# Performance work log

Measured on AMD Instinct MI355X. Metric: run time of the kernel, lower is better.

The kernel has to match this reference:

```python
import jax, jax.numpy as jnp
import numpy as np

HIDDEN = 1024
NUM_HEADS = 16
HEAD_SIZE = HIDDEN // NUM_HEADS
B, S = 2, 2048


def setup_inputs() -> dict:
    key = jax.random.key(0)
    k_x, k_wqkv, k_bqkv, k_wo, k_bo = jax.random.split(key, 5)
    x = jax.random.normal(k_x, (B, S, HIDDEN), dtype=jnp.float32)
    # Dense kernels, fan-in scaled like lecun_normal init
    Wqkv = jax.random.normal(k_wqkv, (HIDDEN, 3 * HIDDEN), dtype=jnp.float32) / np.sqrt(HIDDEN)
    bqkv = jnp.zeros((3 * HIDDEN,), dtype=jnp.float32)
    Wo = jax.random.normal(k_wo, (HIDDEN, HIDDEN), dtype=jnp.float32) / np.sqrt(HIDDEN)
    bo = jnp.zeros((HIDDEN,), dtype=jnp.float32)
    return {"x": x, "Wqkv": Wqkv, "bqkv": bqkv, "Wo": Wo, "bo": bo}


def reference(x, Wqkv, bqkv, Wo, bo):
    b, s, h = x.shape
    qkv = jnp.einsum('bsh,hf->bsf', x, Wqkv) + bqkv          # [b, s, 3*h]
    qkv = qkv.reshape(b, s, 3, NUM_HEADS, HEAD_SIZE)
    q, k, v = qkv[:, :, 0], qkv[:, :, 1], qkv[:, :, 2]        # [b, s, nh, hd]
    scale = 1.0 / np.sqrt(HEAD_SIZE)
    scores = jnp.einsum('bqhd,bkhd->bhqk', q, k) * scale      # [b, nh, s, s]
    weights = jax.nn.softmax(scores, axis=-1)
    attn = jnp.einsum('bhqk,bkhd->bqhd', weights, v)          # [b, s, nh, hd]
    attn = attn.reshape(b, s, h)
    return jnp.einsum('bsh,hf->bsf', attn, Wo) + bo
```

## Files before the change

kernel.cpp:

```cpp
#include <hip/hip_runtime.h>
#include <hip/hip_bf16.h>

#define HIDDEN 1024
#define NH 16
#define BATCH 2
#define SEQ 2048

typedef __attribute__((ext_vector_type(8))) short bf16x8;
typedef __attribute__((ext_vector_type(4))) float f32x4;

__device__ __forceinline__ ushort f2bf(float f) {
    __hip_bfloat16 h = __float2bfloat16(f);
    return *reinterpret_cast<ushort*>(&h);
}
__device__ __forceinline__ float fexp2(float x) {
#if __has_builtin(__builtin_amdgcn_exp2f)
    return __builtin_amdgcn_exp2f(x);
#else
    return exp2f(x);
#endif
}
__device__ __forceinline__ uint pack_bf_trunc(float a, float b) {
    return __builtin_amdgcn_perm(__float_as_uint(b), __float_as_uint(a), 0x07060302u);
}

__device__ __forceinline__ void async_copy16(const ushort* g, ushort* l) {
    __builtin_amdgcn_global_load_lds((const __attribute__((address_space(1))) void*)g,
                                     (__attribute__((address_space(3))) void*)l,
                                     16, 0, 0);
}

__global__ void prep_kernel(const float* __restrict__ x,
                            const float* __restrict__ Wqkv,
                            const float* __restrict__ Wo,
                            ushort* __restrict__ xb,
                            ushort* __restrict__ Wt,
                            ushort* __restrict__ WoT)
{
    __shared__ float t[32][33];
    const int bid = blockIdx.x;
    const int tid = threadIdx.x;

    if (bid < 4096) {
        int i = (bid * 256 + tid) * 4;
        float4 v = *(const float4*)(x + i);
        ushort4 w;
        w.x = f2bf(v.x); w.y = f2bf(v.y); w.z = f2bf(v.z); w.w = f2bf(v.w);
        *(ushort4*)(xb + i) = w;
        return;
    }
    const int r = tid >> 3;
    const int c = (tid & 7) * 4;
    if (bid < 7168) {
        int tt = bid - 4096;
        int k0 = (tt & 31) * 32;
        int n0 = (tt >> 5) * 32;
        const int N = 3 * HIDDEN, K = HIDDEN;
        float4 v = *(const float4*)(Wqkv + (size_t)(k0 + r) * N + n0 + c);
        t[r][c] = v.x; t[r][c + 1] = v.y; t[r][c + 2] = v.z; t[r][c + 3] = v.w;
        __syncthreads();
        ushort4 w;
        w.x = f2bf(t[c + 0][r]); w.y = f2bf(t[c + 1][r]);
        w.z = f2bf(t[c + 2][r]); w.w = f2bf(t[c + 3][r]);
        *(ushort4*)(Wt + (size_t)(n0 + r) * K + k0 + c) = w;
    } else {
        int tt = bid - 7168;
        int k0 = (tt & 31) * 32;
        int n0 = (tt >> 5) * 32;
        const int N = HIDDEN, K = HIDDEN;
        float4 v = *(const float4*)(Wo + (size_t)(k0 + r) * N + n0 + c);
        t[r][c] = v.x; t[r][c + 1] = v.y; t[r][c + 2] = v.z; t[r][c + 3] = v.w;
        __syncthreads();
        ushort4 w;
        w.x = f2bf(t[c + 0][r]); w.y = f2bf(t[c + 1][r]);
        w.z = f2bf(t[c + 2][r]); w.w = f2bf(t[c + 3][r]);
        *(ushort4*)(WoT + (size_t)(n0 + r) * K + k0 + c) = w;
    }
}

__global__ __launch_bounds__(256, 3)
void gemm_mfma_bf16_kernel(const ushort* __restrict__ A,
                           const ushort* __restrict__ Bt,
                           const float* __restrict__ bias,
                           ushort* __restrict__ C, int N,
                           int qscale_cols, float qscale,
                           ushort* __restrict__ vtg, int vt_mode)
{
    constexpr int K = 1024;
    __shared__ ushort As[128 * 64];
    __shared__ ushort Bs[128 * 64];

    const int tid  = threadIdx.x;
    const int wave = tid >> 6;
    const int lane = tid & 63;
    const int l16  = lane & 15;
    const int quad = lane >> 4;
    const int wm = wave & 1, wn = wave >> 1;

    const int bm = blockIdx.y * 128;
    const int bn = blockIdx.x * 128;

    const int srow = lane >> 3;
    const int lblk = (lane & 7) ^ srow;
    const ushort* Ag = A  + (size_t)(bm + wave * 32 + srow) * K + lblk * 8;
    const ushort* Bg = Bt + (size_t)(bn + wave * 32 + srow) * K + lblk * 8;
    ushort* Asl = As + wave * 32 * 64;
    ushort* Bsl = Bs + wave * 32 * 64;

    f32x4 acc[4][4];
    #pragma unroll
    for (int i = 0; i < 4; i++)
        #pragma unroll
        for (int j = 0; j < 4; j++) acc[i][j] = (f32x4){0.f, 0.f, 0.f, 0.f};

    for (int k0 = 0; k0 < K; k0 += 64) {
        __syncthreads();
        #pragma unroll
        for (int t = 0; t < 4; t++) {
            async_copy16(Ag + (size_t)t * 8 * K + k0, Asl + t * 8 * 64);
            async_copy16(Bg + (size_t)t * 8 * K + k0, Bsl + t * 8 * 64);
        }
        __syncthreads();

        #pragma unroll
        for (int s = 0; s < 2; s++) {
            bf16x8 af[4], bfr[4];
            #pragma unroll
            for (int i = 0; i < 4; i++) {
                int m = wm * 64 + i * 16 + l16;
                int n = wn * 64 + i * 16 + l16;
                af[i]  = *(const bf16x8*)&As[m * 64 + (((s * 4 + quad) ^ (m & 7)) << 3)];
                bfr[i] = *(const bf16x8*)&Bs[n * 64 + (((s * 4 + quad) ^ (n & 7)) << 3)];
            }
            #pragma unroll
            for (int i = 0; i < 4; i++)
                #pragma unroll
                for (int j = 0; j < 4; j++)
                    acc[i][j] = __builtin_amdgcn_mfma_f32_16x16x32_bf16(af[i], bfr[j], acc[i][j], 0, 0, 0);
        }
    }

    #pragma unroll
    for (int j = 0; j < 4; j++) {
        int col = bn + wn * 64 + j * 16 + l16;
        float bv = bias[col];
        if (vt_mode && col >= 2048) {
            int dfull = col - 2048;
            int hh = dfull >> 6, dd = dfull & 63;
            int bb = bm >> 11;
            int sb = ((bm & 2047) + wm * 64) >> 6;
            ushort tmp[16];
            #pragma unroll
            for (int i = 0; i < 4; i++)
                #pragma unroll
                for (int r = 0; r < 4; r++)
                    tmp[r * 4 + i] = f2bf(acc[i][j][r] + bv);
            ushort* dst = vtg + ((size_t)((bb * NH + hh) * 64 + dd)) * SEQ
                          + sb * 64 + quad * 16;
            *(uint4*)dst = *(const uint4*)tmp;
            *(uint4*)(dst + 8) = *(const uint4*)(tmp + 8);
        } else {
            float s = (col < qscale_cols) ? qscale : 1.0f;
            #pragma unroll
            for (int i = 0; i < 4; i++) {
                int row0 = bm + wm * 64 + i * 16 + quad * 4;
                #pragma unroll
                for (int r = 0; r < 4; r++)
                    C[(size_t)(row0 + r) * N + col] = f2bf((acc[i][j][r] + bv) * s);
            }
        }
    }
}

__global__ __launch_bounds__(256, 4)
void gemm_out_kernel(const ushort* __restrict__ A,
                     const ushort* __restrict__ Bt,
                     const float* __restrict__ bias,
                     float* __restrict__ C)
{
    constexpr int K = 1024, N = 1024;
    __shared__ ushort As[128 * 64];
    __shared__ ushort Bs[64 * 64];

    const int tid  = threadIdx.x;
    const int wave = tid >> 6;
    const int lane = tid & 63;
    const int l16  = lane & 15;
    const int quad = lane >> 4;
    const int wm = wave & 1, wn = wave >> 1;

    const int bm = blockIdx.y * 128;
    const int bn = blockIdx.x * 64;

    const int srow = lane >> 3;
    const int lblk = (lane & 7) ^ srow;
    const ushort* Ag = A  + (size_t)(bm + wave * 32 + srow) * K + lblk * 8;
    const ushort* Bg = Bt + (size_t)(bn + wave * 16 + srow) * K + lblk * 8;
    ushort* Asl = As + wave * 32 * 64;
    ushort* Bsl = Bs + wave * 16 * 64;

    f32x4 acc[4][2];
    #pragma unroll
    for (int i = 0; i < 4; i++)
        #pragma unroll
        for (int j = 0; j < 2; j++) acc[i][j] = (f32x4){0.f, 0.f, 0.f, 0.f};

    for (int k0 = 0; k0 < K; k0 += 64) {
        __syncthreads();
        #pragma unroll
        for (int t = 0; t < 4; t++)
            async_copy16(Ag + (size_t)t * 8 * K + k0, Asl + t * 8 * 64);
        #pragma unroll
        for (int t = 0; t < 2; t++)
            async_copy16(Bg + (size_t)t * 8 * K + k0, Bsl + t * 8 * 64);
        __syncthreads();

        #pragma unroll
        for (int s = 0; s < 2; s++) {
            bf16x8 af[4], bfr[2];
            #pragma unroll
            for (int i = 0; i < 4; i++) {
                int m = wm * 64 + i * 16 + l16;
                af[i] = *(const bf16x8*)&As[m * 64 + (((s * 4 + quad) ^ (m & 7)) << 3)];
            }
            #pragma unroll
            for (int j = 0; j < 2; j++) {
                int n = wn * 32 + j * 16 + l16;
                bfr[j] = *(const bf16x8*)&Bs[n * 64 + (((s * 4 + quad) ^ (n & 7)) << 3)];
            }
            #pragma unroll
            for (int i = 0; i < 4; i++)
                #pragma unroll
                for (int j = 0; j < 2; j++)
                    acc[i][j] = __builtin_amdgcn_mfma_f32_16x16x32_bf16(af[i], bfr[j], acc[i][j], 0, 0, 0);
        }
    }

    #pragma unroll
    for (int j = 0; j < 2; j++) {
        int col = bn + wn * 32 + j * 16 + l16;
        float bv = bias[col];
        #pragma unroll
        for (int i = 0; i < 4; i++) {
            int row0 = bm + wm * 64 + i * 16 + quad * 4;
            #pragma unroll
            for (int r = 0; r < 4; r++)
                C[(size_t)(row0 + r) * N + col] = acc[i][j][r] + bv;
        }
    }
}

__global__ __launch_bounds__(256, 2)
void attn_mfma_v6_kernel(const ushort* __restrict__ qkvb,
                         const ushort* __restrict__ vtg,
                         ushort* __restrict__ attn)
{
    __shared__ __align__(16) ushort smem[34816];

    const int tid  = threadIdx.x;
    const int wave = tid >> 6;
    const int qg   = wave & 1;
    const int kh   = wave >> 1;
    const int lane = tid & 63;
    const int l16  = lane & 15;
    const int quad = lane >> 4;

    const int qb = blockIdx.x & 15;
    const int bh = blockIdx.x >> 4;
    const int h  = bh & (NH - 1);
    const int b  = bh >> 4;

    const int qbase = qb * 128 + qg * 64;
    const int hoff  = h * 64;

    ushort* KsH = smem + kh * 4096;
    ushort* VsH = smem + 8192 + kh * 4096;
    ushort* Psw = smem + 16384 + wave * 4608;

    bf16x8 a_q[4][2];
    #pragma unroll
    for (int mg = 0; mg < 4; mg++) {
        int qrow = b * SEQ + qbase + mg * 16 + l16;
        const ushort* qp = qkvb + (size_t)qrow * 3072 + hoff + quad * 8;
        a_q[mg][0] = *(const bf16x8*)qp;
        a_q[mg][1] = *(const bf16x8*)(qp + 32);
    }

    f32x4 o[4][4];
    f32x4 lacc[4];
    #pragma unroll
    for (int mg = 0; mg < 4; mg++) {
        lacc[mg] = (f32x4){0.f, 0.f, 0.f, 0.f};
        #pragma unroll
        for (int nt = 0; nt < 4; nt++) o[mg][nt] = (f32x4){0.f, 0.f, 0.f, 0.f};
    }

    bf16x8 b_ones;
    #pragma unroll
    for (int j = 0; j < 8; j++) b_ones[j] = (short)0x3f80;

    const ushort* kvb    = qkvb + (size_t)b * SEQ * 3072;
    const ushort* vtg_bh = vtg + (size_t)((b * NH + h) * 64) * SEQ;

    const int srow8 = lane >> 3;
    const int gblk  = ((lane & 7) ^ srow8) << 3;
    const ushort* kg = kvb + (size_t)(kh * 1024 + qg * 32 + srow8) * 3072 + 1024 + hoff + gblk;
    const ushort* vg = vtg_bh + (size_t)(qg * 32 + srow8) * SEQ + kh * 1024 + gblk;

    for (int t = 0; t < 16; t++) {
        const int k0 = t * 64;
        __syncthreads();
        #pragma unroll
        for (int c = 0; c < 4; c++) {
            async_copy16(kg + (size_t)(k0 + c * 8) * 3072, KsH + (qg * 32 + c * 8) * 64);
            async_copy16(vg + (size_t)(c * 8) * SEQ + k0,  VsH + (qg * 32 + c * 8) * 64);
        }
        __syncthreads();

        f32x4 sc[4][4];
        #pragma unroll
        for (int nt = 0; nt < 4; nt++) {
            int key = nt * 16 + l16;
            bf16x8 bk0 = *(const bf16x8*)&KsH[key * 64 + ((quad ^ (key & 7)) << 3)];
            bf16x8 bk1 = *(const bf16x8*)&KsH[key * 64 + (((4 + quad) ^ (key & 7)) << 3)];
            #pragma unroll
            for (int mg = 0; mg < 4; mg++) {
                f32x4 a = (f32x4){0.f, 0.f, 0.f, 0.f};
                a = __builtin_amdgcn_mfma_f32_16x16x32_bf16(a_q[mg][0], bk0, a, 0, 0, 0);
                a = __builtin_amdgcn_mfma_f32_16x16x32_bf16(a_q[mg][1], bk1, a, 0, 0, 0);
                sc[mg][nt] = a;
            }
        }

        #pragma unroll
        for (int mg = 0; mg < 4; mg++) {
            #pragma unroll
            for (int r = 0; r < 4; r++) {
                int q = mg * 16 + quad * 4 + r;
                uint2 pk2;
                pk2.x = pack_bf_trunc(fexp2(sc[mg][0][r]), fexp2(sc[mg][1][r]));
                pk2.y = pack_bf_trunc(fexp2(sc[mg][2][r]), fexp2(sc[mg][3][r]));
                *(uint2*)&Psw[q * 72 + l16 * 4] = pk2;
            }
        }

        asm volatile("s_waitcnt lgkmcnt(0)" ::: "memory");

        #pragma unroll
        for (int mg = 0; mg < 4; mg++) {
            bf16x8 ap0 = *(const bf16x8*)&Psw[(mg * 16 + l16) * 72 + quad * 8];
            bf16x8 ap1 = *(const bf16x8*)&Psw[(mg * 16 + l16) * 72 + 32 + quad * 8];
            #pragma unroll
            for (int nt = 0; nt < 4; nt++) {
                int d = nt * 16 + l16;
                bf16x8 bv0 = *(const bf16x8*)&VsH[d * 64 + ((quad ^ (d & 7)) << 3)];
                bf16x8 bv1 = *(const bf16x8*)&VsH[d * 64 + (((4 + quad) ^ (d & 7)) << 3)];
                o[mg][nt] = __builtin_amdgcn_mfma_f32_16x16x32_bf16(ap0, bv0, o[mg][nt], 0, 0, 0);
                o[mg][nt] = __builtin_amdgcn_mfma_f32_16x16x32_bf16(ap1, bv1, o[mg][nt], 0, 0, 0);
            }
            lacc[mg] = __builtin_amdgcn_mfma_f32_16x16x32_bf16(ap0, b_ones, lacc[mg], 0, 0, 0);
            lacc[mg] = __builtin_amdgcn_mfma_f32_16x16x32_bf16(ap1, b_ones, lacc[mg], 0, 0, 0);
        }
    }

    __syncthreads();
    float* osc = (float*)smem;
    float* lsc = (float*)(smem + 16384);
    const int ob = qg * 4096;
    const int lb = qg * 64;
    if (kh == 1) {
        #pragma unroll
        for (int mg = 0; mg < 4; mg++) {
            #pragma unroll
            for (int nt = 0; nt < 4; nt++)
                *(f32x4*)&osc[ob + ((mg * 4 + nt) * 4 + quad) * 64 + l16 * 4] = o[mg][nt];
            if (l16 == 0) *(f32x4*)&lsc[lb + (mg * 4 + quad) * 4] = lacc[mg];
        }
    }
    __syncthreads();
    if (kh == 0) {
        #pragma unroll
        for (int mg = 0; mg < 4; mg++) {
            #pragma unroll
            for (int nt = 0; nt < 4; nt++)
                o[mg][nt] += *(const f32x4*)&osc[ob + ((mg * 4 + nt) * 4 + quad) * 64 + l16 * 4];
            lacc[mg] += *(const f32x4*)&lsc[lb + (mg * 4 + quad) * 4];
        }
        #pragma unroll
        for (int mg = 0; mg < 4; mg++) {
            #pragma unroll
            for (int r = 0; r < 4; r++) {
                float inv = 1.f / lacc[mg][r];
                int row = b * SEQ + qbase + mg * 16 + quad * 4 + r;
                size_t base = (size_t)row * HIDDEN + hoff + l16;
                #pragma unroll
                for (int nt = 0; nt < 4; nt++)
                    attn[base + nt * 16] = f2bf(o[mg][nt][r] * inv);
            }
        }
    }
}

__global__ __launch_bounds__(512, 4)
void attn_mfma_fb_kernel(const ushort* __restrict__ qkvb,
                         ushort* __restrict__ attn)
{
    __shared__ __align__(16) ushort smem[34816];

    const int tid   = threadIdx.x;
    const int wave  = tid >> 6;
    const int wavel = wave & 3;
    const int kh    = wave >> 2;
    const int lane  = tid & 63;
    const int l16   = lane & 15;
    const int quad  = lane >> 4;

    const int qb = blockIdx.x & 15;
    const int bh = blockIdx.x >> 4;
    const int h  = bh & (NH - 1);
    const int b  = bh >> 4;

    const int qbase = qb * 128;
    const int hoff  = h * 64;

    ushort* KsH = smem + kh * 4096;
    ushort* VsH = smem + 8192 + kh * 4096;
    ushort* Psw = smem + 16384 + wave * 2304;

    bf16x8 a_q[2][2];
    #pragma unroll
    for (int mg = 0; mg < 2; mg++) {
        int qrow = b * SEQ + qbase + wavel * 32 + mg * 16 + l16;
        const ushort* qp = qkvb + (size_t)qrow * 3072 + hoff + quad * 8;
        a_q[mg][0] = *(const bf16x8*)qp;
        a_q[mg][1] = *(const bf16x8*)(qp + 32);
    }

    f32x4 o[2][4];
    f32x4 lacc[2];
    #pragma unroll
    for (int mg = 0; mg < 2; mg++) {
        lacc[mg] = (f32x4){0.f, 0.f, 0.f, 0.f};
        #pragma unroll
        for (int nt = 0; nt < 4; nt++) o[mg][nt] = (f32x4){0.f, 0.f, 0.f, 0.f};
    }

    bf16x8 b_ones;
    #pragma unroll
    for (int j = 0; j < 8; j++) b_ones[j] = (short)0x3f80;

    const ushort* kvb = qkvb + (size_t)b * SEQ * 3072;

    for (int t = 0; t < 16; t++) {
        const int k0 = t * 64;
        __syncthreads();
        {
            const int tl = tid & 255;
            #pragma unroll
            for (int i = 0; i < 2; i++) {
                int key = (tl >> 3) + 32 * i;
                int blk = tl & 7;
                const ushort* ksrc = kvb + (size_t)(kh * 1024 + k0 + key) * 3072 + 1024 + hoff + blk * 8;
                uint4 kv = *(const uint4*)ksrc;
                *(uint4*)&KsH[key * 64 + ((blk ^ (key & 7)) << 3)] = kv;
                uint4 vv = *(const uint4*)(ksrc + 1024);
                const ushort* vpp = (const ushort*)&vv;
                int pk_ = (key & 15) * 4 + (key >> 4);
                #pragma unroll
                for (int j = 0; j < 8; j++) {
                    int d = blk * 8 + j;
                    VsH[d * 64 + (((pk_ >> 3) ^ (d & 7)) << 3) + (pk_ & 7)] = vpp[j];
                }
            }
        }
        __syncthreads();

        f32x4 sc[2][4];
        #pragma unroll
        for (int nt = 0; nt < 4; nt++) {
            int key = nt * 16 + l16;
            bf16x8 bk0 = *(const bf16x8*)&KsH[key * 64 + ((quad ^ (key & 7)) << 3)];
            bf16x8 bk1 = *(const bf16x8*)&KsH[key * 64 + (((4 + quad) ^ (key & 7)) << 3)];
            #pragma unroll
            for (int mg = 0; mg < 2; mg++) {
                f32x4 a = (f32x4){0.f, 0.f, 0.f, 0.f};
                a = __builtin_amdgcn_mfma_f32_16x16x32_bf16(a_q[mg][0], bk0, a, 0, 0, 0);
                a = __builtin_amdgcn_mfma_f32_16x16x32_bf16(a_q[mg][1], bk1, a, 0, 0, 0);
                sc[mg][nt] = a;
            }
        }

        #pragma unroll
        for (int mg = 0; mg < 2; mg++) {
            #pragma unroll
            for (int r = 0; r < 4; r++) {
                int q = mg * 16 + quad * 4 + r;
                uint2 pk2;
                pk2.x = pack_bf_trunc(fexp2(sc[mg][0][r]), fexp2(sc[mg][1][r]));
                pk2.y = pack_bf_trunc(fexp2(sc[mg][2][r]), fexp2(sc[mg][3][r]));
                *(uint2*)&Psw[q * 72 + l16 * 4] = pk2;
            }
        }

        asm volatile("s_waitcnt lgkmcnt(0)" ::: "memory");
        bf16x8 a_p[2][2];
        #pragma unroll
        for (int mg = 0; mg < 2; mg++) {
            a_p[mg][0] = *(const bf16x8*)&Psw[(mg * 16 + l16) * 72 + quad * 8];
            a_p[mg][1] = *(const bf16x8*)&Psw[(mg * 16 + l16) * 72 + 32 + quad * 8];
        }

        #pragma unroll
        for (int nt = 0; nt < 4; nt++) {
            int d = nt * 16 + l16;
            bf16x8 bv0 = *(const bf16x8*)&VsH[d * 64 + ((quad ^ (d & 7)) << 3)];
            bf16x8 bv1 = *(const bf16x8*)&VsH[d * 64 + (((4 + quad) ^ (d & 7)) << 3)];
            #pragma unroll
            for (int mg = 0; mg < 2; mg++) {
                o[mg][nt] = __builtin_amdgcn_mfma_f32_16x16x32_bf16(a_p[mg][0], bv0, o[mg][nt], 0, 0, 0);
                o[mg][nt] = __builtin_amdgcn_mfma_f32_16x16x32_bf16(a_p[mg][1], bv1, o[mg][nt], 0, 0, 0);
            }
        }
        #pragma unroll
        for (int mg = 0; mg < 2; mg++) {
            lacc[mg] = __builtin_amdgcn_mfma_f32_16x16x32_bf16(a_p[mg][0], b_ones, lacc[mg], 0, 0, 0);
            lacc[mg] = __builtin_amdgcn_mfma_f32_16x16x32_bf16(a_p[mg][1], b_ones, lacc[mg], 0, 0, 0);
        }
    }

    __syncthreads();
    float* osc = (float*)smem;
    float* lsc = (float*)(smem + 16384);
    const int fo = wavel * 2048 + quad * 64 + l16 * 4;
    const int fl = wavel * 512 + quad * 64 + l16 * 4;
    if (kh == 1) {
        #pragma unroll
        for (int mg = 0; mg < 2; mg++) {
            #pragma unroll
            for (int nt = 0; nt < 4; nt++)
                *(f32x4*)&osc[fo + (mg * 4 + nt) * 256] = o[mg][nt];
            *(f32x4*)&lsc[fl + mg * 256] = lacc[mg];
        }
    }
    __syncthreads();
    if (kh == 0) {
        #pragma unroll
        for (int mg = 0; mg < 2; mg++) {
            #pragma unroll
            for (int nt = 0; nt < 4; nt++)
                o[mg][nt] += *(const f32x4*)&osc[fo + (mg * 4 + nt) * 256];
            lacc[mg] += *(const f32x4*)&lsc[fl + mg * 256];
        }
        #pragma unroll
        for (int mg = 0; mg < 2; mg++) {
            #pragma unroll
            for (int r = 0; r < 4; r++) {
                float inv = 1.f / lacc[mg][r];
                int row = b * SEQ + qbase + wavel * 32 + mg * 16 + quad * 4 + r;
                size_t base = (size_t)row * HIDDEN + hoff + l16;
                #pragma unroll
                for (int nt = 0; nt < 4; nt++)
                    attn[base + nt * 16] = f2bf(o[mg][nt][r] * inv);
            }
        }
    }
}

extern "C" void kernel_launch(void* const* d_in, const int* in_sizes, int n_in,
                              void* d_out, int out_size, void* d_ws, size_t ws_size,
                              hipStream_t stream) {
    const float* x    = (const float*)d_in[0];
    const float* Wqkv = (const float*)d_in[1];
    const float* bqkv = (const float*)d_in[2];
    const float* Wo   = (const float*)d_in[3];
    const float* bo   = (const float*)d_in[4];
    float* out = (float*)d_out;

    const int M = BATCH * SEQ;
    const size_t MB = 1024 * 1024;

    char* ws = (char*)d_ws;
    ushort* qkvb = (ushort*)ws;
    ushort* attn = (ushort*)(ws + 24 * MB);
    ushort* xb   = (ushort*)(ws + 24 * MB);
    ushort* Wt   = (ushort*)(ws + 32 * MB);
    ushort* WoT  = (ushort*)(ws + 38 * MB);
    ushort* vtg  = (ushort*)(ws + 40 * MB);
    const int use_vtg = (ws_size >= 48 * MB) ? 1 : 0;

    const float qscale = 0.125f * 1.44269504088896f;

    prep_kernel<<<8192, 256, 0, stream>>>(x, Wqkv, Wo, xb, Wt, WoT);

    {
        dim3 grid((3 * HIDDEN) / 128, M / 128);
        gemm_mfma_bf16_kernel<<<grid, 256, 0, stream>>>(xb, Wt, bqkv, qkvb,
                                                        3 * HIDDEN, HIDDEN, qscale,
                                                        vtg, use_vtg);
    }

    if (use_vtg) {
        attn_mfma_v6_kernel<<<BATCH * NH * (SEQ / 128), 256, 0, stream>>>(
            qkvb, vtg, attn);
    } else {
        attn_mfma_fb_kernel<<<BATCH * NH * (SEQ / 128), 512, 0, stream>>>(
            qkvb, attn);
    }

    {
        dim3 grid(HIDDEN / 64, M / 128);
        gemm_out_kernel<<<grid, 256, 0, stream>>>(attn, WoT, bo, out);
    }
}
```

Measured before the change: 175.2 us.

## Prefetch next K/V tile into registers during compute and remap block order

Replaces the per-iteration async global-to-LDS copy with a register prefetch of the next K/V tile issued before the MFMA work, then stored to shared memory after a barrier, so global latency overlaps compute. Also remaps blockIdx so consecutive blocks cover different batch-heads for the same query block, changing L2 locality and CU spread. This raises register pressure (8 uint4 per thread) and keeps two barriers per iteration. It also assumes the async-copy store layout matches lane*8 addressing.

```diff
diff --git a/kernel.cpp b/kernel.cpp
--- a/kernel.cpp
+++ b/kernel.cpp
@@ -251,7 +251,7 @@
 }
 
 __global__ __launch_bounds__(256, 2)
-void attn_mfma_v6_kernel(const ushort* __restrict__ qkvb,
+void attn_mfma_v7_kernel(const ushort* __restrict__ qkvb,
                          const ushort* __restrict__ vtg,
                          ushort* __restrict__ attn)
 {
@@ -265,8 +265,9 @@
     const int l16  = lane & 15;
     const int quad = lane >> 4;
 
-    const int qb = blockIdx.x & 15;
-    const int bh = blockIdx.x >> 4;
+    const int obid = blockIdx.x;
+    const int qb = (obid >> 3) & 15;
+    const int bh = (obid & 7) * 4 + (obid >> 7);
     const int h  = bh & (NH - 1);
     const int b  = bh >> 4;
 
@@ -307,15 +308,24 @@
     const ushort* kg = kvb + (size_t)(kh * 1024 + qg * 32 + srow8) * 3072 + 1024 + hoff + gblk;
     const ushort* vg = vtg_bh + (size_t)(qg * 32 + srow8) * SEQ + kh * 1024 + gblk;
 
+    #pragma unroll
+    for (int c = 0; c < 4; c++) {
+        async_copy16(kg + (size_t)(c * 8) * 3072, KsH + (qg * 32 + c * 8) * 64);
+        async_copy16(vg + (size_t)(c * 8) * SEQ,  VsH + (qg * 32 + c * 8) * 64);
+    }
+    __syncthreads();
+
+    uint4 kpre[4], vpre[4];
+
     for (int t = 0; t < 16; t++) {
-        const int k0 = t * 64;
-        __syncthreads();
-        #pragma unroll
-        for (int c = 0; c < 4; c++) {
-            async_copy16(kg + (size_t)(k0 + c * 8) * 3072, KsH + (qg * 32 + c * 8) * 64);
-            async_copy16(vg + (size_t)(c * 8) * SEQ + k0,  VsH + (qg * 32 + c * 8) * 64);
-        }
-        __syncthreads();
+        if (t < 15) {
+            const int k0n = (t + 1) * 64;
+            #pragma unroll
+            for (int c = 0; c < 4; c++) {
+                kpre[c] = *(const uint4*)(kg + (size_t)(k0n + c * 8) * 3072);
+                vpre[c] = *(const uint4*)(vg + (size_t)(c * 8) * SEQ + k0n);
+            }
+        }
 
         f32x4 sc[4][4];
         #pragma unroll
@@ -360,6 +370,16 @@
             }
             lacc[mg] = __builtin_amdgcn_mfma_f32_16x16x32_bf16(ap0, b_ones, lacc[mg], 0, 0, 0);
             lacc[mg] = __builtin_amdgcn_mfma_f32_16x16x32_bf16(ap1, b_ones, lacc[mg], 0, 0, 0);
+        }
+
+        __syncthreads();
+        if (t < 15) {
+            #pragma unroll
+            for (int c = 0; c < 4; c++) {
+                *(uint4*)(KsH + (qg * 32 + c * 8) * 64 + lane * 8) = kpre[c];
+                *(uint4*)(VsH + (qg * 32 + c * 8) * 64 + lane * 8) = vpre[c];
+            }
+            __syncthreads();
         }
     }
 
@@ -600,7 +620,7 @@
     }
 
     if (use_vtg) {
-        attn_mfma_v6_kernel<<<BATCH * NH * (SEQ / 128), 256, 0, stream>>>(
+        attn_mfma_v7_kernel<<<BATCH * NH * (SEQ / 128), 256, 0, stream>>>(
             qkvb, vtg, attn);
     } else {
         attn_mfma_fb_kernel<<<BATCH * NH * (SEQ / 128), 512, 0, stream>>>(
```

Result: slower. 213.2 us (+21.7%).
